# Kernel optimization log

Hardware: AMD Instinct MI355X
Metric: run time of the kernel (lower is better)

Reference implementation:

```python
import jax, jax.numpy as jnp
import numpy as np

B, T, C, H = 2, 2048, 1024, 16
D = C // H

def setup_inputs() -> dict:
    key = jax.random.key(0)
    ks = jax.random.split(key, 8)
    s = 1.0 / np.sqrt(C)
    return {
        "x": jax.random.normal(ks[0], (B, T, C), dtype=jnp.float32),
        "Wk": jax.random.normal(ks[1], (C, C), dtype=jnp.float32) * s,
        "Wq": jax.random.normal(ks[2], (C, C), dtype=jnp.float32) * s,
        "bq": jax.random.normal(ks[3], (C,), dtype=jnp.float32) * 0.02,
        "Wv": jax.random.normal(ks[4], (C, C), dtype=jnp.float32) * s,
        "bv": jax.random.normal(ks[5], (C,), dtype=jnp.float32) * 0.02,
        "Wo": jax.random.normal(ks[6], (C, C), dtype=jnp.float32) * s,
        "bo": jax.random.normal(ks[7], (C,), dtype=jnp.float32) * 0.02,
    }

def reference(x, Wk, Wq, bq, Wv, bv, Wo, bo):
    b, t, c = x.shape
    # projections (key has no bias, matching nn.Linear(bias=False))
    q = (x @ Wq.T + bq).reshape(b, t, H, D).transpose(0, 2, 1, 3)  # [B,H,T,D]
    k = (x @ Wk.T).reshape(b, t, H, D).transpose(0, 2, 1, 3)
    v = (x @ Wv.T + bv).reshape(b, t, H, D).transpose(0, 2, 1, 3)
    scale = D ** -0.5
    attn = jnp.einsum('bhqd,bhkd->bhqk', q, k) * scale  # [B,H,T,T]
    causal = jnp.tril(jnp.ones((t, t), dtype=bool))
    attn = jnp.where(causal[None, None], attn, -jnp.inf)
    attn = jax.nn.softmax(attn, axis=-1)
    y = jnp.einsum('bhqk,bhkd->bhqd', attn, v)  # [B,H,T,D]
    y = y.transpose(0, 2, 1, 3).reshape(b, t, c)
    return y @ Wo.T + bo
```

## Files before the change

### kernel.cpp

```cpp
#include <hip/hip_runtime.h>
#include <hip/hip_bf16.h>
#include <stdint.h>

#define B_ 2
#define T_ 2048
#define C_ 1024
#define H_ 16
#define D_ 64
#define M_ (B_ * T_)

typedef __bf16 bf16x8 __attribute__((ext_vector_type(8)));
typedef float f32x4 __attribute__((ext_vector_type(4)));
typedef float f32x16 __attribute__((ext_vector_type(16)));

__device__ inline void gload_lds16(const void* g, void* l) {
  __builtin_amdgcn_global_load_lds(
      (const __attribute__((address_space(1))) void*)g,
      (__attribute__((address_space(3))) void*)l, 16, 0, 0);
}

__global__ __launch_bounds__(256) void cvt_all(
    const float* __restrict__ x, const float* __restrict__ Wq,
    const float* __restrict__ Wk, const float* __restrict__ Wv,
    const float* __restrict__ Wo, __hip_bfloat16* __restrict__ xb,
    __hip_bfloat16* __restrict__ wqb, __hip_bfloat16* __restrict__ wkb,
    __hip_bfloat16* __restrict__ wvb, __hip_bfloat16* __restrict__ wob) {
  size_t t = (size_t)blockIdx.x * 256 + threadIdx.x;
  size_t e = t * 4;
  const float* src;
  __hip_bfloat16* dst;
  size_t off;
  if (e < 4194304) {
    src = x; dst = xb; off = e;
  } else {
    size_t u = e - 4194304;
    int seg = (int)(u >> 20);
    off = u & 1048575;
    src = (seg == 0) ? Wq : (seg == 1) ? Wk : (seg == 2) ? Wv : Wo;
    dst = (seg == 0) ? wqb : (seg == 1) ? wkb : (seg == 2) ? wvb : wob;
  }
  float4 v = *(const float4*)(src + off);
  union { __hip_bfloat16 h[4]; ushort4 u4; } cv;
  cv.h[0] = __float2bfloat16(v.x);
  cv.h[1] = __float2bfloat16(v.y);
  cv.h[2] = __float2bfloat16(v.z);
  cv.h[3] = __float2bfloat16(v.w);
  *(ushort4*)(dst + off) = cv.u4;
}

__global__ __launch_bounds__(256) void gemm_qkv(
    const __hip_bfloat16* __restrict__ X,
    const __hip_bfloat16* __restrict__ Wq,
    const __hip_bfloat16* __restrict__ Wk,
    const __hip_bfloat16* __restrict__ Wv,
    const float* __restrict__ bq, const float* __restrict__ bv,
    __hip_bfloat16* __restrict__ Qo, __hip_bfloat16* __restrict__ Ko,
    __hip_bfloat16* __restrict__ VTo) {
  const int z = blockIdx.z;
  const int bx = ((blockIdx.x & 3) << 3) | (blockIdx.x >> 2);
  const __hip_bfloat16* Amat;
  const __hip_bfloat16* Bmat;
  int bm, bn;
  if (z == 2) {
    Amat = Wv; Bmat = X; bm = blockIdx.y; bn = bx;
  } else {
    Amat = X; Bmat = (z == 0) ? Wq : Wk; bm = bx; bn = blockIdx.y;
  }

  const int tid = threadIdx.x;
  const int w = tid >> 6, lane = tid & 63;
  const int wr = w >> 1, wc = w & 1;
  const int lrow = lane & 15, lk = (lane >> 4) * 8;

  __shared__ __hip_bfloat16 As[128 * 32];
  __shared__ __hip_bfloat16 Bs[128 * 32];

  f32x4 acc[4][4];
#pragma unroll
  for (int m = 0; m < 4; ++m)
#pragma unroll
    for (int n = 0; n < 4; ++n) acc[m][n] = (f32x4){0.f, 0.f, 0.f, 0.f};

  for (int k0 = 0; k0 < C_; k0 += 32) {
#pragma unroll
    for (int it = 0; it < 2; ++it) {
      int e = it * 2048 + w * 512 + lane * 8;
      int row = e >> 5, col = e & 31;
      gload_lds16(Amat + (size_t)(bm * 128 + row) * C_ + k0 + col, &As[e]);
      gload_lds16(Bmat + (size_t)(bn * 128 + row) * C_ + k0 + col, &Bs[e]);
    }
    asm volatile("s_waitcnt vmcnt(0)" ::: "memory");
    __syncthreads();

    bf16x8 af[4], bfr[4];
#pragma unroll
    for (int m = 0; m < 4; ++m)
      af[m] = *(const bf16x8*)&As[(wr * 64 + m * 16 + lrow) * 32 + lk];
#pragma unroll
    for (int n = 0; n < 4; ++n)
      bfr[n] = *(const bf16x8*)&Bs[(wc * 64 + n * 16 + lrow) * 32 + lk];
#pragma unroll
    for (int m = 0; m < 4; ++m)
#pragma unroll
      for (int n = 0; n < 4; ++n)
        acc[m][n] = __builtin_amdgcn_mfma_f32_16x16x32_bf16(af[m], bfr[n],
                                                            acc[m][n], 0, 0, 0);
    __syncthreads();
  }

#pragma unroll
  for (int m = 0; m < 4; ++m) {
#pragma unroll
    for (int n = 0; n < 4; ++n) {
      f32x4 v = acc[m][n];
      int rowm = bm * 128 + wr * 64 + m * 16 + (lane >> 4) * 4;
      int coln = bn * 128 + wc * 64 + n * 16 + (lane & 15);
      if (z == 2) {
        int b = coln >> 11, tl = coln & 2047;
#pragma unroll
        for (int r = 0; r < 4; ++r) {
          int rc = rowm + r;
          int h = rc >> 6, d = rc & 63;
          VTo[(((size_t)(b * H_ + h)) * D_ + d) * T_ + tl] =
              __float2bfloat16(v[r] + bv[rc]);
        }
      } else {
        float bb = (z == 0) ? bq[coln] : 0.f;
        float sc = (z == 0) ? 0.18033688011112042f : 1.0f;
        int h = coln >> 6, d = coln & 63;
        __hip_bfloat16* Out = (z == 0) ? Qo : Ko;
#pragma unroll
        for (int r = 0; r < 4; ++r) {
          int row = rowm + r;
          int b = row >> 11, t = row & 2047;
          Out[(((size_t)(b * H_ + h)) * T_ + t) * D_ + d] =
              __float2bfloat16((v[r] + bb) * sc);
        }
      }
    }
  }
}

__global__ __launch_bounds__(256) void gemm_out(
    const __hip_bfloat16* __restrict__ X,
    const __hip_bfloat16* __restrict__ W,
    const float* __restrict__ bias, float* __restrict__ Out) {
  const int bm = ((blockIdx.x & 3) << 3) | (blockIdx.x >> 2);
  const int bn = blockIdx.y;
  const int tid = threadIdx.x;
  const int w = tid >> 6, lane = tid & 63;
  const int wr = w >> 1, wc = w & 1;
  const int lrow = lane & 15, lk = (lane >> 4) * 8;

  __shared__ __hip_bfloat16 As[128 * 32];
  __shared__ __hip_bfloat16 Bs[128 * 32];

  f32x4 acc[4][4];
#pragma unroll
  for (int m = 0; m < 4; ++m)
#pragma unroll
    for (int n = 0; n < 4; ++n) acc[m][n] = (f32x4){0.f, 0.f, 0.f, 0.f};

  for (int k0 = 0; k0 < C_; k0 += 32) {
#pragma unroll
    for (int it = 0; it < 2; ++it) {
      int e = it * 2048 + w * 512 + lane * 8;
      int row = e >> 5, col = e & 31;
      gload_lds16(X + (size_t)(bm * 128 + row) * C_ + k0 + col, &As[e]);
      gload_lds16(W + (size_t)(bn * 128 + row) * C_ + k0 + col, &Bs[e]);
    }
    asm volatile("s_waitcnt vmcnt(0)" ::: "memory");
    __syncthreads();

    bf16x8 af[4], bfr[4];
#pragma unroll
    for (int m = 0; m < 4; ++m)
      af[m] = *(const bf16x8*)&As[(wr * 64 + m * 16 + lrow) * 32 + lk];
#pragma unroll
    for (int n = 0; n < 4; ++n)
      bfr[n] = *(const bf16x8*)&Bs[(wc * 64 + n * 16 + lrow) * 32 + lk];
#pragma unroll
    for (int m = 0; m < 4; ++m)
#pragma unroll
      for (int n = 0; n < 4; ++n)
        acc[m][n] = __builtin_amdgcn_mfma_f32_16x16x32_bf16(af[m], bfr[n],
                                                            acc[m][n], 0, 0, 0);
    __syncthreads();
  }

#pragma unroll
  for (int m = 0; m < 4; ++m) {
#pragma unroll
    for (int n = 0; n < 4; ++n) {
      f32x4 v = acc[m][n];
      int coln = bn * 128 + wc * 64 + n * 16 + (lane & 15);
      float bb = bias[coln];
#pragma unroll
      for (int r = 0; r < 4; ++r) {
        int row = bm * 128 + wr * 64 + m * 16 + (lane >> 4) * 4 + r;
        Out[(size_t)row * C_ + coln] = v[r] + bb;
      }
    }
  }
}

#define MASKV_ -1e30f
#define MFLOOR_ -30000.0f
#define THR2_ 11.54f

__global__ __launch_bounds__(512, 2) void attn_fwd(
    const __hip_bfloat16* __restrict__ Q, const __hip_bfloat16* __restrict__ K,
    const __hip_bfloat16* __restrict__ VT, __hip_bfloat16* __restrict__ Y) {
  const int bh = blockIdx.x;
  const int j = blockIdx.y;
  const int tid = threadIdx.x;
  const int wid = tid >> 6, lane = tid & 63;
  const int g = wid >> 2, wq = wid & 3;
  const int hi = lane >> 5, q32 = lane & 31;
  const size_t base = (size_t)bh * T_ * D_;
  const int b = bh >> 4, hh = bh & 15;

  __shared__ __hip_bfloat16 Ks[2][2][64][64];
  __shared__ __hip_bfloat16 Vts[2][2][64][64];
  __shared__ float Sml[2][4][2][32];
  __shared__ float Om[4][32][68];

  const int gt = tid & 255;
  const int srow = gt >> 3, scnk = gt & 7;
  const int swz = (scnk ^ (srow & 7)) * 8;

#define STAGE(buf, kt)                                                      \
  {                                                                         \
    _Pragma("unroll") for (int h2 = 0; h2 < 2; ++h2) {                      \
      int row = srow + 32 * h2;                                             \
      gload_lds16(K + base + (size_t)((kt)*64 + row) * D_ + swz,            \
                  &Ks[g][(buf)][row][scnk * 8]);                            \
      gload_lds16(VT + base + (size_t)row * T_ + (kt)*64 + swz,             \
                  &Vts[g][(buf)][row][scnk * 8]);                           \
    }                                                                       \
  }

  for (int ph = 0; ph < 2; ++ph) {
    const int qt = ph ? (15 - j) : j;
    const int qg = qt * 128 + wq * 32 + q32;

    bf16x8 qf[4];
#pragma unroll
    for (int dk = 0; dk < 4; ++dk)
      qf[dk] = *(const bf16x8*)&Q[base + (size_t)qg * D_ + dk * 16 + hi * 8];

    f32x16 o0 = {}, o1 = {};
    float m_run = MFLOOR_, l_run = 0.f;

    STAGE(0, g);
    asm volatile("s_waitcnt vmcnt(0)" ::: "memory");
    __syncthreads();

    int cur = 0;
    for (int s = 0; s <= qt; ++s) {
      const int kt = 2 * s + g;
      if (s < qt) STAGE(cur ^ 1, 2 * (s + 1) + g);

      f32x16 st0 = {}, st1 = {};
      __builtin_amdgcn_s_setprio(1);
#pragma unroll
      for (int dk = 0; dk < 4; ++dk) {
        int off = (dk * 16 + hi * 8) ^ ((lane & 7) << 3);
        bf16x8 a0 = *(const bf16x8*)&Ks[g][cur][q32][off];
        bf16x8 a1 = *(const bf16x8*)&Ks[g][cur][q32 + 32][off];
        st0 = __builtin_amdgcn_mfma_f32_32x32x16_bf16(a0, qf[dk], st0, 0, 0, 0);
        st1 = __builtin_amdgcn_mfma_f32_32x32x16_bf16(a1, qf[dk], st1, 0, 0, 0);
      }
      __builtin_amdgcn_s_setprio(0);

      float sc[32];
#pragma unroll
      for (int r = 0; r < 16; ++r) {
        sc[r] = st0[r];
        sc[16 + r] = st1[r];
      }
      if (s == qt) {
#pragma unroll
        for (int r = 0; r < 16; ++r) {
          int kvl = (r & 3) + 8 * (r >> 2) + 4 * hi;
          if (kt * 64 + kvl > qg) sc[r] = MASKV_;
          if (kt * 64 + 32 + kvl > qg) sc[16 + r] = MASKV_;
        }
      }
      float mt = sc[0];
#pragma unroll
      for (int r = 1; r < 32; ++r) mt = fmaxf(mt, sc[r]);
      mt = fmaxf(mt, __shfl_xor(mt, 32));
      if (__any(mt - m_run > THR2_)) {
        float m_new = fmaxf(m_run, mt);
        float alpha = __builtin_exp2f(m_run - m_new);
        m_run = m_new;
        l_run *= alpha;
#pragma unroll
        for (int r = 0; r < 16; ++r) {
          o0[r] *= alpha;
          o1[r] *= alpha;
        }
      }
      float ls = 0.f;
#pragma unroll
      for (int r = 0; r < 32; ++r) {
        float p = __builtin_exp2f(sc[r] - m_run);
        sc[r] = p;
        ls += p;
      }
      ls += __shfl_xor(ls, 32);
      l_run += ls;

      __builtin_amdgcn_s_setprio(1);
#pragma unroll
      for (int ks = 0; ks < 4; ++ks) {
        union { unsigned w[4]; bf16x8 v; } pa;
        unsigned A, Bb;
        asm("v_cvt_pk_bf16_f32 %0, %1, %2"
            : "=v"(A) : "v"(sc[ks * 8 + 0]), "v"(sc[ks * 8 + 1]));
        asm("v_cvt_pk_bf16_f32 %0, %1, %2"
            : "=v"(Bb) : "v"(sc[ks * 8 + 4]), "v"(sc[ks * 8 + 5]));
        asm volatile("v_permlane32_swap_b32 %0, %1" : "+v"(A), "+v"(Bb));
        pa.w[0] = A;
        pa.w[2] = Bb;
        asm("v_cvt_pk_bf16_f32 %0, %1, %2"
            : "=v"(A) : "v"(sc[ks * 8 + 2]), "v"(sc[ks * 8 + 3]));
        asm("v_cvt_pk_bf16_f32 %0, %1, %2"
            : "=v"(Bb) : "v"(sc[ks * 8 + 6]), "v"(sc[ks * 8 + 7]));
        asm volatile("v_permlane32_swap_b32 %0, %1" : "+v"(A), "+v"(Bb));
        pa.w[1] = A;
        pa.w[3] = Bb;

        int voff = (ks * 16 + hi * 8) ^ ((lane & 7) << 3);
        bf16x8 v0 = *(const bf16x8*)&Vts[g][cur][q32][voff];
        bf16x8 v1 = *(const bf16x8*)&Vts[g][cur][q32 + 32][voff];
        o0 = __builtin_amdgcn_mfma_f32_32x32x16_bf16(v0, pa.v, o0, 0, 0, 0);
        o1 = __builtin_amdgcn_mfma_f32_32x32x16_bf16(v1, pa.v, o1, 0, 0, 0);
      }
      __builtin_amdgcn_s_setprio(0);

      asm volatile("s_waitcnt vmcnt(0)" ::: "memory");
      __syncthreads();
      cur ^= 1;
    }

    if (lane < 32) {
      Sml[g][wq][0][lane] = m_run;
      Sml[g][wq][1][lane] = l_run;
    }
    __syncthreads();
    float mo = Sml[1 - g][wq][0][q32];
    float lo_ = Sml[1 - g][wq][1][q32];
    float mstar = fmaxf(m_run, mo);
    float f = __builtin_exp2f(m_run - mstar);
    float fo = __builtin_exp2f(mo - mstar);
    float lstar = l_run * f + lo_ * fo;

    if (g == 1) {
#pragma unroll
      for (int dt = 0; dt < 2; ++dt) {
#pragma unroll
        for (int grp = 0; grp < 4; ++grp) {
          int dbase = grp * 8 + hi * 4 + dt * 32;
          float4 t4;
          t4.x = (dt ? o1[grp * 4 + 0] : o0[grp * 4 + 0]) * f;
          t4.y = (dt ? o1[grp * 4 + 1] : o0[grp * 4 + 1]) * f;
          t4.z = (dt ? o1[grp * 4 + 2] : o0[grp * 4 + 2]) * f;
          t4.w = (dt ? o1[grp * 4 + 3] : o0[grp * 4 + 3]) * f;
          *(float4*)&Om[wq][q32][dbase] = t4;
        }
      }
    }
    __syncthreads();
    if (g == 0) {
      float inv = 1.0f / lstar;
#pragma unroll
      for (int dt = 0; dt < 2; ++dt) {
#pragma unroll
        for (int grp = 0; grp < 4; ++grp) {
          int dbase = grp * 8 + hi * 4 + dt * 32;
          float4 m4 = *(float4*)&Om[wq][q32][dbase];
          union { __hip_bfloat16 h4[4]; ushort4 u; } pk;
          float e0 = (dt ? o1[grp * 4 + 0] : o0[grp * 4 + 0]) * f + m4.x;
          float e1 = (dt ? o1[grp * 4 + 1] : o0[grp * 4 + 1]) * f + m4.y;
          float e2 = (dt ? o1[grp * 4 + 2] : o0[grp * 4 + 2]) * f + m4.z;
          float e3 = (dt ? o1[grp * 4 + 3] : o0[grp * 4 + 3]) * f + m4.w;
          pk.h4[0] = __float2bfloat16(e0 * inv);
          pk.h4[1] = __float2bfloat16(e1 * inv);
          pk.h4[2] = __float2bfloat16(e2 * inv);
          pk.h4[3] = __float2bfloat16(e3 * inv);
          *(ushort4*)&Y[((size_t)b * T_ + qg) * C_ + hh * 64 + dbase] = pk.u;
        }
      }
    }
    __syncthreads();
  }
}

extern "C" void kernel_launch(void* const* d_in, const int* in_sizes, int n_in,
                              void* d_out, int out_size, void* d_ws,
                              size_t ws_size, hipStream_t stream) {
  const float* x = (const float*)d_in[0];
  const float* Wk = (const float*)d_in[1];
  const float* Wq = (const float*)d_in[2];
  const float* bq = (const float*)d_in[3];
  const float* Wv = (const float*)d_in[4];
  const float* bv = (const float*)d_in[5];
  const float* Wo = (const float*)d_in[6];
  const float* bo = (const float*)d_in[7];
  float* out = (float*)d_out;

  char* ws = (char*)d_ws;
  __hip_bfloat16* xb = (__hip_bfloat16*)(ws);
  __hip_bfloat16* wqb = (__hip_bfloat16*)(ws + (8ull << 20));
  __hip_bfloat16* wkb = (__hip_bfloat16*)(ws + (10ull << 20));
  __hip_bfloat16* wvb = (__hip_bfloat16*)(ws + (12ull << 20));
  __hip_bfloat16* wob = (__hip_bfloat16*)(ws + (14ull << 20));
  __hip_bfloat16* Qb = (__hip_bfloat16*)(ws + (16ull << 20));
  __hip_bfloat16* Kb = (__hip_bfloat16*)(ws + (24ull << 20));
  __hip_bfloat16* VTb = (__hip_bfloat16*)(ws + (32ull << 20));
  __hip_bfloat16* Yb = (__hip_bfloat16*)(ws + (40ull << 20));

  cvt_all<<<8192, 256, 0, stream>>>(x, Wq, Wk, Wv, Wo, xb, wqb, wkb, wvb, wob);
  gemm_qkv<<<dim3(32, 8, 3), 256, 0, stream>>>(xb, wqb, wkb, wvb, bq, bv, Qb,
                                               Kb, VTb);
  attn_fwd<<<dim3(32, 8), 512, 0, stream>>>(Qb, Kb, VTb, Yb);
  gemm_out<<<dim3(32, 8), 256, 0, stream>>>(Yb, wob, bo, out);
}
```

Baseline: 111.9 us.

## Double-buffer GEMM LDS tiles and triple-buffer attention K/V staging

Both projection GEMMs (QKV and output) now use two LDS buffers, so the next K-slice is prefetched with global_load_lds while MFMAs run on the current slice. The attention kernel moves from double to triple buffering of K/Vt tiles, keeping two stages in flight and waiting with vmcnt(4) instead of draining every load. Shared memory is repacked into one raw buffer where Om aliases the K region, which raises per-block LDS use and may reduce occupancy at two blocks per CU.

```diff
diff --git a/kernel.cpp b/kernel.cpp
--- a/kernel.cpp
+++ b/kernel.cpp
@@ -72,8 +72,8 @@
   const int wr = w >> 1, wc = w & 1;
   const int lrow = lane & 15, lk = (lane >> 4) * 8;
 
-  __shared__ __hip_bfloat16 As[128 * 32];
-  __shared__ __hip_bfloat16 Bs[128 * 32];
+  __shared__ __hip_bfloat16 As[2][128 * 32];
+  __shared__ __hip_bfloat16 Bs[2][128 * 32];
 
   f32x4 acc[4][4];
 #pragma unroll
@@ -81,31 +81,42 @@
 #pragma unroll
     for (int n = 0; n < 4; ++n) acc[m][n] = (f32x4){0.f, 0.f, 0.f, 0.f};
 
-  for (int k0 = 0; k0 < C_; k0 += 32) {
-#pragma unroll
-    for (int it = 0; it < 2; ++it) {
-      int e = it * 2048 + w * 512 + lane * 8;
-      int row = e >> 5, col = e & 31;
-      gload_lds16(Amat + (size_t)(bm * 128 + row) * C_ + k0 + col, &As[e]);
-      gload_lds16(Bmat + (size_t)(bn * 128 + row) * C_ + k0 + col, &Bs[e]);
-    }
-    asm volatile("s_waitcnt vmcnt(0)" ::: "memory");
-    __syncthreads();
+#define GSTAGE_Q(buf, k0)                                                   \
+  {                                                                         \
+    _Pragma("unroll") for (int it = 0; it < 2; ++it) {                      \
+      int e = it * 2048 + w * 512 + lane * 8;                               \
+      int row = e >> 5, col = e & 31;                                       \
+      gload_lds16(Amat + (size_t)(bm * 128 + row) * C_ + (k0) + col,        \
+                  &As[(buf)][e]);                                           \
+      gload_lds16(Bmat + (size_t)(bn * 128 + row) * C_ + (k0) + col,        \
+                  &Bs[(buf)][e]);                                           \
+    }                                                                       \
+  }
+
+  GSTAGE_Q(0, 0);
+  asm volatile("s_waitcnt vmcnt(0)" ::: "memory");
+  __syncthreads();
+
+  int buf = 0;
+  for (int kk = 0; kk < 32; ++kk) {
+    if (kk + 1 < 32) GSTAGE_Q(buf ^ 1, (kk + 1) * 32);
 
     bf16x8 af[4], bfr[4];
 #pragma unroll
     for (int m = 0; m < 4; ++m)
-      af[m] = *(const bf16x8*)&As[(wr * 64 + m * 16 + lrow) * 32 + lk];
+      af[m] = *(const bf16x8*)&As[buf][(wr * 64 + m * 16 + lrow) * 32 + lk];
 #pragma unroll
     for (int n = 0; n < 4; ++n)
-      bfr[n] = *(const bf16x8*)&Bs[(wc * 64 + n * 16 + lrow) * 32 + lk];
+      bfr[n] = *(const bf16x8*)&Bs[buf][(wc * 64 + n * 16 + lrow) * 32 + lk];
 #pragma unroll
     for (int m = 0; m < 4; ++m)
 #pragma unroll
       for (int n = 0; n < 4; ++n)
         acc[m][n] = __builtin_amdgcn_mfma_f32_16x16x32_bf16(af[m], bfr[n],
                                                             acc[m][n], 0, 0, 0);
-    __syncthreads();
+    asm volatile("s_waitcnt vmcnt(0)" ::: "memory");
+    __syncthreads();
+    buf ^= 1;
   }
 
 #pragma unroll
@@ -152,8 +163,8 @@
   const int wr = w >> 1, wc = w & 1;
   const int lrow = lane & 15, lk = (lane >> 4) * 8;
 
-  __shared__ __hip_bfloat16 As[128 * 32];
-  __shared__ __hip_bfloat16 Bs[128 * 32];
+  __shared__ __hip_bfloat16 As[2][128 * 32];
+  __shared__ __hip_bfloat16 Bs[2][128 * 32];
 
   f32x4 acc[4][4];
 #pragma unroll
@@ -161,31 +172,42 @@
 #pragma unroll
     for (int n = 0; n < 4; ++n) acc[m][n] = (f32x4){0.f, 0.f, 0.f, 0.f};
 
-  for (int k0 = 0; k0 < C_; k0 += 32) {
-#pragma unroll
-    for (int it = 0; it < 2; ++it) {
-      int e = it * 2048 + w * 512 + lane * 8;
-      int row = e >> 5, col = e & 31;
-      gload_lds16(X + (size_t)(bm * 128 + row) * C_ + k0 + col, &As[e]);
-      gload_lds16(W + (size_t)(bn * 128 + row) * C_ + k0 + col, &Bs[e]);
-    }
-    asm volatile("s_waitcnt vmcnt(0)" ::: "memory");
-    __syncthreads();
+#define GSTAGE_O(buf, k0)                                                   \
+  {                                                                         \
+    _Pragma("unroll") for (int it = 0; it < 2; ++it) {                      \
+      int e = it * 2048 + w * 512 + lane * 8;                               \
+      int row = e >> 5, col = e & 31;                                       \
+      gload_lds16(X + (size_t)(bm * 128 + row) * C_ + (k0) + col,           \
+                  &As[(buf)][e]);                                           \
+      gload_lds16(W + (size_t)(bn * 128 + row) * C_ + (k0) + col,           \
+                  &Bs[(buf)][e]);                                           \
+    }                                                                       \
+  }
+
+  GSTAGE_O(0, 0);
+  asm volatile("s_waitcnt vmcnt(0)" ::: "memory");
+  __syncthreads();
+
+  int buf = 0;
+  for (int kk = 0; kk < 32; ++kk) {
+    if (kk + 1 < 32) GSTAGE_O(buf ^ 1, (kk + 1) * 32);
 
     bf16x8 af[4], bfr[4];
 #pragma unroll
     for (int m = 0; m < 4; ++m)
-      af[m] = *(const bf16x8*)&As[(wr * 64 + m * 16 + lrow) * 32 + lk];
+      af[m] = *(const bf16x8*)&As[buf][(wr * 64 + m * 16 + lrow) * 32 + lk];
 #pragma unroll
     for (int n = 0; n < 4; ++n)
-      bfr[n] = *(const bf16x8*)&Bs[(wc * 64 + n * 16 + lrow) * 32 + lk];
+      bfr[n] = *(const bf16x8*)&Bs[buf][(wc * 64 + n * 16 + lrow) * 32 + lk];
 #pragma unroll
     for (int m = 0; m < 4; ++m)
 #pragma unroll
       for (int n = 0; n < 4; ++n)
         acc[m][n] = __builtin_amdgcn_mfma_f32_16x16x32_bf16(af[m], bfr[n],
                                                             acc[m][n], 0, 0, 0);
-    __syncthreads();
+    asm volatile("s_waitcnt vmcnt(0)" ::: "memory");
+    __syncthreads();
+    buf ^= 1;
   }
 
 #pragma unroll
@@ -220,10 +242,11 @@
   const size_t base = (size_t)bh * T_ * D_;
   const int b = bh >> 4, hh = bh & 15;
 
-  __shared__ __hip_bfloat16 Ks[2][2][64][64];
-  __shared__ __hip_bfloat16 Vts[2][2][64][64];
-  __shared__ float Sml[2][4][2][32];
-  __shared__ float Om[4][32][68];
+  __shared__ __align__(16) char smem[98304 + 2048];
+  auto Ks = (__hip_bfloat16(*)[3][64][64])(smem);
+  auto Vts = (__hip_bfloat16(*)[3][64][64])(smem + 49152);
+  float* Sml = (float*)(smem + 98304);
+  float(*Om)[32][68] = (float(*)[32][68])(smem);
 
   const int gt = tid & 255;
   const int srow = gt >> 3, scnk = gt & 7;
@@ -253,13 +276,19 @@
     float m_run = MFLOOR_, l_run = 0.f;
 
     STAGE(0, g);
-    asm volatile("s_waitcnt vmcnt(0)" ::: "memory");
-    __syncthreads();
-
-    int cur = 0;
+    if (qt > 0) {
+      STAGE(1, 2 + g);
+      asm volatile("s_waitcnt vmcnt(4)" ::: "memory");
+    } else {
+      asm volatile("s_waitcnt vmcnt(0)" ::: "memory");
+    }
+    __syncthreads();
+
     for (int s = 0; s <= qt; ++s) {
       const int kt = 2 * s + g;
-      if (s < qt) STAGE(cur ^ 1, 2 * (s + 1) + g);
+      const int cur = s % 3;
+      const bool issue = (s + 2 <= qt);
+      if (issue) STAGE((s + 2) % 3, 2 * (s + 2) + g);
 
       f32x16 st0 = {}, st1 = {};
       __builtin_amdgcn_s_setprio(1);
@@ -340,18 +369,21 @@
       }
       __builtin_amdgcn_s_setprio(0);
 
-      asm volatile("s_waitcnt vmcnt(0)" ::: "memory");
+      if (issue) {
+        asm volatile("s_waitcnt vmcnt(4)" ::: "memory");
+      } else {
+        asm volatile("s_waitcnt vmcnt(0)" ::: "memory");
+      }
       __syncthreads();
-      cur ^= 1;
     }
 
     if (lane < 32) {
-      Sml[g][wq][0][lane] = m_run;
-      Sml[g][wq][1][lane] = l_run;
-    }
-    __syncthreads();
-    float mo = Sml[1 - g][wq][0][q32];
-    float lo_ = Sml[1 - g][wq][1][q32];
+      Sml[((g * 4 + wq) * 2 + 0) * 32 + lane] = m_run;
+      Sml[((g * 4 + wq) * 2 + 1) * 32 + lane] = l_run;
+    }
+    __syncthreads();
+    float mo = Sml[(((1 - g) * 4 + wq) * 2 + 0) * 32 + q32];
+    float lo_ = Sml[(((1 - g) * 4 + wq) * 2 + 1) * 32 + q32];
     float mstar = fmaxf(m_run, mo);
     float f = __builtin_exp2f(m_run - mstar);
     float fo = __builtin_exp2f(mo - mstar);
```

Result: slower. 118.0 us (+5.5%).

## Rewrite attention to load K/V straight into registers without LDS or split-KV

Applied to the files above, without the earlier changes.

The attention kernel no longer stages K and V^T tiles through LDS with async global-to-LDS loads, double buffering and block barriers. Each wave now loads its own K and V fragments directly from global memory into registers, prefetching the next tile while computing the current one. The two-group KV split and its LDS merge are gone. The grid becomes one 256-thread block per (query tile, head), ordered longest tile first instead of pairing tiles for balance. This removes barriers and LDS traffic, but each of the four waves now fetches the same K/V from global memory or cache, and register pressure rises.

```diff
diff --git a/kernel.cpp b/kernel.cpp
--- a/kernel.cpp
+++ b/kernel.cpp
@@ -208,193 +208,151 @@
 #define MFLOOR_ -30000.0f
 #define THR2_ 11.54f
 
-__global__ __launch_bounds__(512, 2) void attn_fwd(
+__global__ __launch_bounds__(256, 3) void attn_fwd(
     const __hip_bfloat16* __restrict__ Q, const __hip_bfloat16* __restrict__ K,
     const __hip_bfloat16* __restrict__ VT, __hip_bfloat16* __restrict__ Y) {
-  const int bh = blockIdx.x;
-  const int j = blockIdx.y;
-  const int tid = threadIdx.x;
-  const int wid = tid >> 6, lane = tid & 63;
-  const int g = wid >> 2, wq = wid & 3;
+  const int bid = blockIdx.x;
+  const int qt = 15 - (bid >> 5);
+  const int bh = bid & 31;
+  const int lane = threadIdx.x & 63;
+  const int wq = threadIdx.x >> 6;
   const int hi = lane >> 5, q32 = lane & 31;
   const size_t base = (size_t)bh * T_ * D_;
   const int b = bh >> 4, hh = bh & 15;
-
-  __shared__ __hip_bfloat16 Ks[2][2][64][64];
-  __shared__ __hip_bfloat16 Vts[2][2][64][64];
-  __shared__ float Sml[2][4][2][32];
-  __shared__ float Om[4][32][68];
-
-  const int gt = tid & 255;
-  const int srow = gt >> 3, scnk = gt & 7;
-  const int swz = (scnk ^ (srow & 7)) * 8;
-
-#define STAGE(buf, kt)                                                      \
-  {                                                                         \
-    _Pragma("unroll") for (int h2 = 0; h2 < 2; ++h2) {                      \
-      int row = srow + 32 * h2;                                             \
-      gload_lds16(K + base + (size_t)((kt)*64 + row) * D_ + swz,            \
-                  &Ks[g][(buf)][row][scnk * 8]);                            \
-      gload_lds16(VT + base + (size_t)row * T_ + (kt)*64 + swz,             \
-                  &Vts[g][(buf)][row][scnk * 8]);                           \
-    }                                                                       \
-  }
-
-  for (int ph = 0; ph < 2; ++ph) {
-    const int qt = ph ? (15 - j) : j;
-    const int qg = qt * 128 + wq * 32 + q32;
-
-    bf16x8 qf[4];
-#pragma unroll
-    for (int dk = 0; dk < 4; ++dk)
-      qf[dk] = *(const bf16x8*)&Q[base + (size_t)qg * D_ + dk * 16 + hi * 8];
-
-    f32x16 o0 = {}, o1 = {};
-    float m_run = MFLOOR_, l_run = 0.f;
-
-    STAGE(0, g);
-    asm volatile("s_waitcnt vmcnt(0)" ::: "memory");
-    __syncthreads();
-
-    int cur = 0;
-    for (int s = 0; s <= qt; ++s) {
-      const int kt = 2 * s + g;
-      if (s < qt) STAGE(cur ^ 1, 2 * (s + 1) + g);
-
-      f32x16 st0 = {}, st1 = {};
-      __builtin_amdgcn_s_setprio(1);
-#pragma unroll
-      for (int dk = 0; dk < 4; ++dk) {
-        int off = (dk * 16 + hi * 8) ^ ((lane & 7) << 3);
-        bf16x8 a0 = *(const bf16x8*)&Ks[g][cur][q32][off];
-        bf16x8 a1 = *(const bf16x8*)&Ks[g][cur][q32 + 32][off];
-        st0 = __builtin_amdgcn_mfma_f32_32x32x16_bf16(a0, qf[dk], st0, 0, 0, 0);
-        st1 = __builtin_amdgcn_mfma_f32_32x32x16_bf16(a1, qf[dk], st1, 0, 0, 0);
+  const int qg = qt * 128 + wq * 32 + q32;
+
+  bf16x8 qf[4];
+#pragma unroll
+  for (int dk = 0; dk < 4; ++dk)
+    qf[dk] = *(const bf16x8*)&Q[base + (size_t)qg * D_ + dk * 16 + hi * 8];
+
+  const __hip_bfloat16* Kr0 = K + base + (size_t)q32 * D_ + hi * 8;
+  const __hip_bfloat16* Kr1 = K + base + (size_t)(q32 + 32) * D_ + hi * 8;
+  const __hip_bfloat16* Vr0 = VT + base + (size_t)q32 * T_ + hi * 8;
+  const __hip_bfloat16* Vr1 = VT + base + (size_t)(q32 + 32) * T_ + hi * 8;
+
+  f32x16 o0 = {}, o1 = {};
+  float m_run = MFLOOR_, l_run = 0.f;
+  const int nkt = 2 * qt + 2;
+
+  bf16x8 k0[4], k1[4], v0[4], v1[4];
+
+#define LOADK(kt)                                                       \
+  {                                                                     \
+    size_t kof = (size_t)(kt) * 64 * D_;                                \
+    _Pragma("unroll") for (int dk = 0; dk < 4; ++dk) {                  \
+      k0[dk] = *(const bf16x8*)&Kr0[kof + dk * 16];                     \
+      k1[dk] = *(const bf16x8*)&Kr1[kof + dk * 16];                     \
+    }                                                                   \
+  }
+#define LOADV(kt)                                                       \
+  {                                                                     \
+    int vof = (kt)*64;                                                  \
+    _Pragma("unroll") for (int ks = 0; ks < 4; ++ks) {                  \
+      v0[ks] = *(const bf16x8*)&Vr0[vof + ks * 16];                     \
+      v1[ks] = *(const bf16x8*)&Vr1[vof + ks * 16];                     \
+    }                                                                   \
+  }
+
+  LOADK(0);
+  LOADV(0);
+
+  for (int kt = 0; kt < nkt; ++kt) {
+    f32x16 st0 = {}, st1 = {};
+    __builtin_amdgcn_s_setprio(1);
+#pragma unroll
+    for (int dk = 0; dk < 4; ++dk) {
+      st0 = __builtin_amdgcn_mfma_f32_32x32x16_bf16(k0[dk], qf[dk], st0, 0, 0, 0);
+      st1 = __builtin_amdgcn_mfma_f32_32x32x16_bf16(k1[dk], qf[dk], st1, 0, 0, 0);
+    }
+    __builtin_amdgcn_s_setprio(0);
+
+    if (kt + 1 < nkt) LOADK(kt + 1);
+
+    float sc[32];
+#pragma unroll
+    for (int r = 0; r < 16; ++r) {
+      sc[r] = st0[r];
+      sc[16 + r] = st1[r];
+    }
+    if (kt >= 2 * qt) {
+#pragma unroll
+      for (int r = 0; r < 16; ++r) {
+        int kvl = (r & 3) + 8 * (r >> 2) + 4 * hi;
+        if (kt * 64 + kvl > qg) sc[r] = MASKV_;
+        if (kt * 64 + 32 + kvl > qg) sc[16 + r] = MASKV_;
       }
-      __builtin_amdgcn_s_setprio(0);
-
-      float sc[32];
+    }
+    float mt = sc[0];
+#pragma unroll
+    for (int r = 1; r < 32; ++r) mt = fmaxf(mt, sc[r]);
+    mt = fmaxf(mt, __shfl_xor(mt, 32));
+    if (__any(mt - m_run > THR2_)) {
+      float m_new = fmaxf(m_run, mt);
+      float alpha = __builtin_exp2f(m_run - m_new);
+      m_run = m_new;
+      l_run *= alpha;
 #pragma unroll
       for (int r = 0; r < 16; ++r) {
-        sc[r] = st0[r];
-        sc[16 + r] = st1[r];
+        o0[r] *= alpha;
+        o1[r] *= alpha;
       }
-      if (s == qt) {
-#pragma unroll
-        for (int r = 0; r < 16; ++r) {
-          int kvl = (r & 3) + 8 * (r >> 2) + 4 * hi;
-          if (kt * 64 + kvl > qg) sc[r] = MASKV_;
-          if (kt * 64 + 32 + kvl > qg) sc[16 + r] = MASKV_;
-        }
-      }
-      float mt = sc[0];
-#pragma unroll
-      for (int r = 1; r < 32; ++r) mt = fmaxf(mt, sc[r]);
-      mt = fmaxf(mt, __shfl_xor(mt, 32));
-      if (__any(mt - m_run > THR2_)) {
-        float m_new = fmaxf(m_run, mt);
-        float alpha = __builtin_exp2f(m_run - m_new);
-        m_run = m_new;
-        l_run *= alpha;
-#pragma unroll
-        for (int r = 0; r < 16; ++r) {
-          o0[r] *= alpha;
-          o1[r] *= alpha;
-        }
-      }
-      float ls = 0.f;
-#pragma unroll
-      for (int r = 0; r < 32; ++r) {
-        float p = __builtin_exp2f(sc[r] - m_run);
-        sc[r] = p;
-        ls += p;
-      }
-      ls += __shfl_xor(ls, 32);
-      l_run += ls;
-
-      __builtin_amdgcn_s_setprio(1);
-#pragma unroll
-      for (int ks = 0; ks < 4; ++ks) {
-        union { unsigned w[4]; bf16x8 v; } pa;
-        unsigned A, Bb;
-        asm("v_cvt_pk_bf16_f32 %0, %1, %2"
-            : "=v"(A) : "v"(sc[ks * 8 + 0]), "v"(sc[ks * 8 + 1]));
-        asm("v_cvt_pk_bf16_f32 %0, %1, %2"
-            : "=v"(Bb) : "v"(sc[ks * 8 + 4]), "v"(sc[ks * 8 + 5]));
-        asm volatile("v_permlane32_swap_b32 %0, %1" : "+v"(A), "+v"(Bb));
-        pa.w[0] = A;
-        pa.w[2] = Bb;
-        asm("v_cvt_pk_bf16_f32 %0, %1, %2"
-            : "=v"(A) : "v"(sc[ks * 8 + 2]), "v"(sc[ks * 8 + 3]));
-        asm("v_cvt_pk_bf16_f32 %0, %1, %2"
-            : "=v"(Bb) : "v"(sc[ks * 8 + 6]), "v"(sc[ks * 8 + 7]));
-        asm volatile("v_permlane32_swap_b32 %0, %1" : "+v"(A), "+v"(Bb));
-        pa.w[1] = A;
-        pa.w[3] = Bb;
-
-        int voff = (ks * 16 + hi * 8) ^ ((lane & 7) << 3);
-        bf16x8 v0 = *(const bf16x8*)&Vts[g][cur][q32][voff];
-        bf16x8 v1 = *(const bf16x8*)&Vts[g][cur][q32 + 32][voff];
-        o0 = __builtin_amdgcn_mfma_f32_32x32x16_bf16(v0, pa.v, o0, 0, 0, 0);
-        o1 = __builtin_amdgcn_mfma_f32_32x32x16_bf16(v1, pa.v, o1, 0, 0, 0);
-      }
-      __builtin_amdgcn_s_setprio(0);
-
-      asm volatile("s_waitcnt vmcnt(0)" ::: "memory");
-      __syncthreads();
-      cur ^= 1;
-    }
-
-    if (lane < 32) {
-      Sml[g][wq][0][lane] = m_run;
-      Sml[g][wq][1][lane] = l_run;
-    }
-    __syncthreads();
-    float mo = Sml[1 - g][wq][0][q32];
-    float lo_ = Sml[1 - g][wq][1][q32];
-    float mstar = fmaxf(m_run, mo);
-    float f = __builtin_exp2f(m_run - mstar);
-    float fo = __builtin_exp2f(mo - mstar);
-    float lstar = l_run * f + lo_ * fo;
-
-    if (g == 1) {
-#pragma unroll
-      for (int dt = 0; dt < 2; ++dt) {
-#pragma unroll
-        for (int grp = 0; grp < 4; ++grp) {
-          int dbase = grp * 8 + hi * 4 + dt * 32;
-          float4 t4;
-          t4.x = (dt ? o1[grp * 4 + 0] : o0[grp * 4 + 0]) * f;
-          t4.y = (dt ? o1[grp * 4 + 1] : o0[grp * 4 + 1]) * f;
-          t4.z = (dt ? o1[grp * 4 + 2] : o0[grp * 4 + 2]) * f;
-          t4.w = (dt ? o1[grp * 4 + 3] : o0[grp * 4 + 3]) * f;
-          *(float4*)&Om[wq][q32][dbase] = t4;
-        }
-      }
-    }
-    __syncthreads();
-    if (g == 0) {
-      float inv = 1.0f / lstar;
-#pragma unroll
-      for (int dt = 0; dt < 2; ++dt) {
-#pragma unroll
-        for (int grp = 0; grp < 4; ++grp) {
-          int dbase = grp * 8 + hi * 4 + dt * 32;
-          float4 m4 = *(float4*)&Om[wq][q32][dbase];
-          union { __hip_bfloat16 h4[4]; ushort4 u; } pk;
-          float e0 = (dt ? o1[grp * 4 + 0] : o0[grp * 4 + 0]) * f + m4.x;
-          float e1 = (dt ? o1[grp * 4 + 1] : o0[grp * 4 + 1]) * f + m4.y;
-          float e2 = (dt ? o1[grp * 4 + 2] : o0[grp * 4 + 2]) * f + m4.z;
-          float e3 = (dt ? o1[grp * 4 + 3] : o0[grp * 4 + 3]) * f + m4.w;
-          pk.h4[0] = __float2bfloat16(e0 * inv);
-          pk.h4[1] = __float2bfloat16(e1 * inv);
-          pk.h4[2] = __float2bfloat16(e2 * inv);
-          pk.h4[3] = __float2bfloat16(e3 * inv);
-          *(ushort4*)&Y[((size_t)b * T_ + qg) * C_ + hh * 64 + dbase] = pk.u;
-        }
-      }
-    }
-    __syncthreads();
+    }
+    float ls = 0.f;
+#pragma unroll
+    for (int r = 0; r < 32; ++r) {
+      float p = __builtin_exp2f(sc[r] - m_run);
+      sc[r] = p;
+      ls += p;
+    }
+    ls += __shfl_xor(ls, 32);
+    l_run += ls;
+
+    __builtin_amdgcn_s_setprio(1);
+#pragma unroll
+    for (int ks = 0; ks < 4; ++ks) {
+      union { unsigned w[4]; bf16x8 v; } pa;
+      unsigned A, Bb;
+      asm("v_cvt_pk_bf16_f32 %0, %1, %2"
+          : "=v"(A) : "v"(sc[ks * 8 + 0]), "v"(sc[ks * 8 + 1]));
+      asm("v_cvt_pk_bf16_f32 %0, %1, %2"
+          : "=v"(Bb) : "v"(sc[ks * 8 + 4]), "v"(sc[ks * 8 + 5]));
+      asm volatile("v_permlane32_swap_b32 %0, %1" : "+v"(A), "+v"(Bb));
+      pa.w[0] = A;
+      pa.w[2] = Bb;
+      asm("v_cvt_pk_bf16_f32 %0, %1, %2"
+          : "=v"(A) : "v"(sc[ks * 8 + 2]), "v"(sc[ks * 8 + 3]));
+      asm("v_cvt_pk_bf16_f32 %0, %1, %2"
+          : "=v"(Bb) : "v"(sc[ks * 8 + 6]), "v"(sc[ks * 8 + 7]));
+      asm volatile("v_permlane32_swap_b32 %0, %1" : "+v"(A), "+v"(Bb));
+      pa.w[1] = A;
+      pa.w[3] = Bb;
+
+      o0 = __builtin_amdgcn_mfma_f32_32x32x16_bf16(v0[ks], pa.v, o0, 0, 0, 0);
+      o1 = __builtin_amdgcn_mfma_f32_32x32x16_bf16(v1[ks], pa.v, o1, 0, 0, 0);
+    }
+    __builtin_amdgcn_s_setprio(0);
+
+    if (kt + 1 < nkt) LOADV(kt + 1);
+  }
+
+  float inv = 1.0f / l_run;
+#pragma unroll
+  for (int dt = 0; dt < 2; ++dt) {
+#pragma unroll
+    for (int grp = 0; grp < 4; ++grp) {
+      int dbase = grp * 8 + hi * 4 + dt * 32;
+      union { __hip_bfloat16 h4[4]; ushort4 u; } pk;
+      float e0 = (dt ? o1[grp * 4 + 0] : o0[grp * 4 + 0]) * inv;
+      float e1 = (dt ? o1[grp * 4 + 1] : o0[grp * 4 + 1]) * inv;
+      float e2 = (dt ? o1[grp * 4 + 2] : o0[grp * 4 + 2]) * inv;
+      float e3 = (dt ? o1[grp * 4 + 3] : o0[grp * 4 + 3]) * inv;
+      pk.h4[0] = __float2bfloat16(e0);
+      pk.h4[1] = __float2bfloat16(e1);
+      pk.h4[2] = __float2bfloat16(e2);
+      pk.h4[3] = __float2bfloat16(e3);
+      *(ushort4*)&Y[((size_t)b * T_ + qg) * C_ + hh * 64 + dbase] = pk.u;
+    }
   }
 }
 
@@ -425,6 +383,6 @@
   cvt_all<<<8192, 256, 0, stream>>>(x, Wq, Wk, Wv, Wo, xb, wqb, wkb, wvb, wob);
   gemm_qkv<<<dim3(32, 8, 3), 256, 0, stream>>>(xb, wqb, wkb, wvb, bq, bv, Qb,
                                                Kb, VTb);
-  attn_fwd<<<dim3(32, 8), 512, 0, stream>>>(Qb, Kb, VTb, Yb);
+  attn_fwd<<<512, 256, 0, stream>>>(Qb, Kb, VTb, Yb);
   gemm_out<<<dim3(32, 8), 256, 0, stream>>>(Yb, wob, bo, out);
 }
```

Result: slower. 157.0 us (+40.3%).

## Triple-buffer K/V tiles in attention and tree-reduce row max and sum

Applied to the files above, without the earlier changes.

Moves the K and V^T shared-memory staging from double to triple buffering, so loads are issued two tiles ahead and the loop waits with a partial vmcnt instead of draining all loads. Shared memory becomes one raw buffer, with the output-merge scratch aliased over the K region. The per-row max and sum reductions become pairwise trees to shorten the dependency chains. The cost is about 98KB of LDS per block, which may lower occupancy below the two blocks per CU the launch bounds ask for.

```diff
diff --git a/kernel.cpp b/kernel.cpp
--- a/kernel.cpp
+++ b/kernel.cpp
@@ -220,10 +220,11 @@
   const size_t base = (size_t)bh * T_ * D_;
   const int b = bh >> 4, hh = bh & 15;
 
-  __shared__ __hip_bfloat16 Ks[2][2][64][64];
-  __shared__ __hip_bfloat16 Vts[2][2][64][64];
-  __shared__ float Sml[2][4][2][32];
-  __shared__ float Om[4][32][68];
+  __shared__ __align__(16) char smem[98304 + 2048];
+  auto Ks = (__hip_bfloat16(*)[3][64][64])(smem);
+  auto Vts = (__hip_bfloat16(*)[3][64][64])(smem + 49152);
+  float* Sml = (float*)(smem + 98304);
+  float(*Om)[32][68] = (float(*)[32][68])(smem);
 
   const int gt = tid & 255;
   const int srow = gt >> 3, scnk = gt & 7;
@@ -253,13 +254,19 @@
     float m_run = MFLOOR_, l_run = 0.f;
 
     STAGE(0, g);
-    asm volatile("s_waitcnt vmcnt(0)" ::: "memory");
-    __syncthreads();
-
-    int cur = 0;
+    if (qt > 0) {
+      STAGE(1, 2 + g);
+      asm volatile("s_waitcnt vmcnt(4)" ::: "memory");
+    } else {
+      asm volatile("s_waitcnt vmcnt(0)" ::: "memory");
+    }
+    __syncthreads();
+
     for (int s = 0; s <= qt; ++s) {
       const int kt = 2 * s + g;
-      if (s < qt) STAGE(cur ^ 1, 2 * (s + 1) + g);
+      const int cur = s % 3;
+      const bool issue = (s + 2 <= qt);
+      if (issue) STAGE((s + 2) % 3, 2 * (s + 2) + g);
 
       f32x16 st0 = {}, st1 = {};
       __builtin_amdgcn_s_setprio(1);
@@ -287,9 +294,15 @@
           if (kt * 64 + 32 + kvl > qg) sc[16 + r] = MASKV_;
         }
       }
-      float mt = sc[0];
-#pragma unroll
-      for (int r = 1; r < 32; ++r) mt = fmaxf(mt, sc[r]);
+      float tm[16];
+#pragma unroll
+      for (int r = 0; r < 16; ++r) tm[r] = fmaxf(sc[r], sc[16 + r]);
+#pragma unroll
+      for (int off2 = 8; off2 > 0; off2 >>= 1)
+#pragma unroll
+        for (int r = 0; r < 8; ++r)
+          if (r < off2) tm[r] = fmaxf(tm[r], tm[r + off2]);
+      float mt = tm[0];
       mt = fmaxf(mt, __shfl_xor(mt, 32));
       if (__any(mt - m_run > THR2_)) {
         float m_new = fmaxf(m_run, mt);
@@ -302,13 +315,17 @@
           o1[r] *= alpha;
         }
       }
-      float ls = 0.f;
-#pragma unroll
-      for (int r = 0; r < 32; ++r) {
-        float p = __builtin_exp2f(sc[r] - m_run);
-        sc[r] = p;
-        ls += p;
-      }
+#pragma unroll
+      for (int r = 0; r < 32; ++r) sc[r] = __builtin_exp2f(sc[r] - m_run);
+      float ts[16];
+#pragma unroll
+      for (int r = 0; r < 16; ++r) ts[r] = sc[r] + sc[16 + r];
+#pragma unroll
+      for (int off2 = 8; off2 > 0; off2 >>= 1)
+#pragma unroll
+        for (int r = 0; r < 8; ++r)
+          if (r < off2) ts[r] = ts[r] + ts[r + off2];
+      float ls = ts[0];
       ls += __shfl_xor(ls, 32);
       l_run += ls;
 
@@ -340,18 +357,21 @@
       }
       __builtin_amdgcn_s_setprio(0);
 
-      asm volatile("s_waitcnt vmcnt(0)" ::: "memory");
+      if (issue) {
+        asm volatile("s_waitcnt vmcnt(4)" ::: "memory");
+      } else {
+        asm volatile("s_waitcnt vmcnt(0)" ::: "memory");
+      }
       __syncthreads();
-      cur ^= 1;
     }
 
     if (lane < 32) {
-      Sml[g][wq][0][lane] = m_run;
-      Sml[g][wq][1][lane] = l_run;
-    }
-    __syncthreads();
-    float mo = Sml[1 - g][wq][0][q32];
-    float lo_ = Sml[1 - g][wq][1][q32];
+      Sml[((g * 4 + wq) * 2 + 0) * 32 + lane] = m_run;
+      Sml[((g * 4 + wq) * 2 + 1) * 32 + lane] = l_run;
+    }
+    __syncthreads();
+    float mo = Sml[(((1 - g) * 4 + wq) * 2 + 0) * 32 + q32];
+    float lo_ = Sml[(((1 - g) * 4 + wq) * 2 + 1) * 32 + q32];
     float mstar = fmaxf(m_run, mo);
     float f = __builtin_exp2f(m_run - mstar);
     float fo = __builtin_exp2f(mo - mstar);
```

Measured after the change: 111.8 us. No clear change (-0.1%).
